# Performance work log

Hardware: AMD Instinct MI355X
Metric: run time of the kernel (lower is better)

The kernel has to match this reference:

```python
import jax, jax.numpy as jnp
import numpy as np

NH, NOPE_D, ROPE_D, V_D, R = 16, 48, 16, 64, 128
EPS = 1e-6

def rms_norm(x, w):
    norm = jax.lax.rsqrt(jnp.mean(jnp.square(x), axis=-1, keepdims=True) + EPS)
    return x * norm * w

def apply_rope(x, cos, sin):
    # x: (..., rope_d); cos/sin broadcastable (..., rope_d//2)
    d = x.shape[-1]
    x1, x2 = x[..., : d // 2], x[..., d // 2 :]
    return jnp.concatenate([x1 * cos - x2 * sin, x2 * cos + x1 * sin], axis=-1)

def setup_inputs() -> dict:
    key = jax.random.key(0)
    ks = jax.random.split(key, 8)
    B, T, D = 2, 2048, 1024
    s = lambda fan_in: 1.0 / np.sqrt(fan_in)
    return {
        "x": jax.random.normal(ks[0], (B, T, D), jnp.float32),
        "cos": jax.random.uniform(ks[1], (T, ROPE_D // 2), jnp.float32),
        "sin": jax.random.uniform(ks[2], (T, ROPE_D // 2), jnp.float32),
        "Wq": jax.random.normal(ks[3], (NH * (NOPE_D + ROPE_D), D), jnp.float32) * s(D),
        "q_norm_w": jnp.ones((NOPE_D + ROPE_D,), jnp.float32),
        "Wkva": jax.random.normal(ks[4], (R + ROPE_D, D), jnp.float32) * s(D),
        "kva_norm_w": jnp.ones((R,), jnp.float32),
        "Wkvb": jax.random.normal(ks[5], (NH * (NOPE_D + V_D), R), jnp.float32) * s(R),
        "Wo": jax.random.normal(ks[6], (D, NH * V_D), jnp.float32) * s(NH * V_D),
    }

def reference(x, cos, sin, Wq, q_norm_w, Wkva, kva_norm_w, Wkvb, Wo):
    B, T, D = x.shape
    # Q path: project, per-head RMSNorm over (nope+rope) dims, split
    q = (x @ Wq.T).reshape(B, T, NH, NOPE_D + ROPE_D)
    q = rms_norm(q, q_norm_w)
    q_nope, q_rope = q[..., :NOPE_D], q[..., NOPE_D:]
    # Low-rank KV path
    kv_a = x @ Wkva.T  # (B,T,R+ROPE_D)
    kv_latent = rms_norm(kv_a[..., :R], kva_norm_w)
    k_rope_raw = kv_a[..., R:]  # (B,T,ROPE_D) shared across heads
    kv_b = (kv_latent @ Wkvb.T).reshape(B, T, NH, NOPE_D + V_D)
    k_nope, v = kv_b[..., :NOPE_D], kv_b[..., NOPE_D:]
    # Decoupled RoPE
    cos_t = cos[None, :T, None, :]  # (1,T,1,rope_d/2)
    sin_t = sin[None, :T, None, :]
    q_rope = apply_rope(q_rope, cos_t, sin_t)
    k_rope = apply_rope(k_rope_raw[:, :, None, :], cos[None, :T, None, :], sin[None, :T, None, :])
    k_rope = jnp.broadcast_to(k_rope, (B, T, NH, ROPE_D))
    q_full = jnp.concatenate([q_nope, q_rope], axis=-1)  # (B,T,NH,64)
    k_full = jnp.concatenate([k_nope, k_rope], axis=-1)
    # Causal attention, scale = 1/sqrt(nope+rope)
    scale = (NOPE_D + ROPE_D) ** -0.5
    scores = jnp.einsum("bqhd,bkhd->bhqk", q_full, k_full) * scale
    causal = jnp.tril(jnp.ones((T, T), bool))
    scores = jnp.where(causal[None, None], scores, -jnp.inf)
    attn = jax.nn.softmax(scores, axis=-1)
    out = jnp.einsum("bhqk,bkhd->bqhd", attn, v).reshape(B, T, NH * V_D)
    return out @ Wo.T
```

## Files before the change

### kernel.cpp

```cpp
#include <hip/hip_runtime.h>
#include <hip/hip_bf16.h>
#include <math.h>

#define NH 16
#define T_ 2048
#define B_ 2
#define D_ 1024
#define EPS 1e-6f

typedef __attribute__((ext_vector_type(8))) short bf16x8;
typedef __attribute__((ext_vector_type(4))) float f32x4;

__device__ __forceinline__ float wred_sum(float v){
  #pragma unroll
  for (int o = 32; o > 0; o >>= 1) v += __shfl_xor(v, o, 64);
  return v;
}

__device__ __forceinline__ unsigned pack_bf16(float a, float b){
  __hip_bfloat162 t = __float22bfloat162_rn(make_float2(a, b));
  unsigned r; __builtin_memcpy(&r, &t, 4); return r;
}

__device__ __forceinline__ void gload_lds16(const void* g, void* l){
  __builtin_amdgcn_global_load_lds((const __attribute__((address_space(1))) void*)g,
                                   (__attribute__((address_space(3))) void*)l, 16, 0, 0);
}

__global__ __launch_bounds__(256)
void cvt5(const float* __restrict__ x, const float* __restrict__ wq,
          const float* __restrict__ wkva, const float* __restrict__ wkvb,
          const float* __restrict__ wo,
          __hip_bfloat16* __restrict__ xb, __hip_bfloat16* __restrict__ wqb,
          __hip_bfloat16* __restrict__ wkvab, __hip_bfloat16* __restrict__ wkvbb,
          __hip_bfloat16* __restrict__ wob)
{
  const int i = blockIdx.x * 256 + threadIdx.x;
  const float* s; __hip_bfloat16* d; size_t soff, doff;
  if      (i < 1048576) { s = x;    d = xb;    soff = doff = i; }
  else if (i < 1310720) { s = wq;   d = wqb;   soff = doff = i - 1048576; }
  else if (i < 1347584) { s = wkva; d = wkvab; soff = doff = i - 1310720; }
  else if (i < 1404928) {
    const int off = i - 1347584;
    const int srow = off >> 5, c4 = off & 31;
    const int h = srow / 112, dd = srow % 112;
    const int drow = (dd < 48) ? (h*48 + dd) : (768 + h*64 + (dd - 48));
    s = wkvb; d = wkvbb; soff = off; doff = (size_t)drow*32 + c4;
  }
  else                  { s = wo;   d = wob;   soff = doff = i - 1404928; }
  float4 v = *(const float4*)(s + soff * 4);
  *(__hip_bfloat162*)(d + doff * 4)     = __float22bfloat162_rn(make_float2(v.x, v.y));
  *(__hip_bfloat162*)(d + doff * 4 + 2) = __float22bfloat162_rn(make_float2(v.z, v.w));
}

template<typename CT>
__global__ __launch_bounds__(256, 2)
void gemm_bt64(const __hip_bfloat16* __restrict__ A, const __hip_bfloat16* __restrict__ W,
               CT* __restrict__ C, int M, int N, int K)
{
  __shared__ __hip_bfloat16 As[2][128 * 64];
  __shared__ __hip_bfloat16 Ws[2][64 * 64];
  const int tid = threadIdx.x;
  const int wv = tid >> 6, lane = tid & 63;
  const int m = lane & 15, quad = lane >> 4;
  const int bm = blockIdx.y * 128, bn = blockIdx.x * 64;

  const __hip_bfloat16* ga[4];
  const __hip_bfloat16* gw[2];
  #pragma unroll
  for (int i = 0; i < 4; i++) {
    const int slot = i*256 + tid;
    const int row = slot >> 3, cb = slot & 7;
    ga[i] = A + (size_t)(bm + row) * K + ((cb ^ (row & 7)) << 3);
  }
  #pragma unroll
  for (int i = 0; i < 2; i++) {
    const int slot = i*256 + tid;
    const int row = slot >> 3, cb = slot & 7;
    int wr = bn + row; if (wr >= N) wr = N - 1;
    gw[i] = W + (size_t)wr * K + ((cb ^ (row & 7)) << 3);
  }
  auto stage = [&](int buf){
    #pragma unroll
    for (int i = 0; i < 4; i++) { gload_lds16(ga[i], &As[buf][(i*256 + wv*64)*8]); ga[i] += 64; }
    #pragma unroll
    for (int i = 0; i < 2; i++) { gload_lds16(gw[i], &Ws[buf][(i*256 + wv*64)*8]); gw[i] += 64; }
  };

  f32x4 acc[2][4];
  #pragma unroll
  for (int mi = 0; mi < 2; mi++)
    #pragma unroll
    for (int nj = 0; nj < 4; nj++) acc[mi][nj] = (f32x4){0.f,0.f,0.f,0.f};

  stage(0);
  const int iters = K >> 6;
  for (int it = 0; it < iters; it++) {
    const int cur = it & 1;
    __syncthreads();
    if (it + 1 < iters) stage(cur ^ 1);
    #pragma unroll
    for (int ks = 0; ks < 2; ks++) {
      const int cb = ((ks*4 + quad) ^ (m & 7)) << 3;
      bf16x8 af[2], wf[4];
      #pragma unroll
      for (int mi = 0; mi < 2; mi++)
        af[mi] = *(const bf16x8*)(&As[cur][(wv*32 + mi*16 + m) * 64 + cb]);
      #pragma unroll
      for (int nj = 0; nj < 4; nj++)
        wf[nj] = *(const bf16x8*)(&Ws[cur][(nj*16 + m) * 64 + cb]);
      #pragma unroll
      for (int mi = 0; mi < 2; mi++)
        #pragma unroll
        for (int nj = 0; nj < 4; nj++)
          acc[mi][nj] = __builtin_amdgcn_mfma_f32_16x16x32_bf16(af[mi], wf[nj], acc[mi][nj], 0, 0, 0);
    }
  }

  #pragma unroll
  for (int mi = 0; mi < 2; mi++)
    #pragma unroll
    for (int nj = 0; nj < 4; nj++) {
      const int col = bn + nj*16 + m;
      if (col < N) {
        #pragma unroll
        for (int r = 0; r < 4; r++) {
          const int row = bm + wv*32 + mi*16 + quad*4 + r;
          if constexpr (sizeof(CT) == 2)
            C[(size_t)row * N + col] = (CT)__float2bfloat16(acc[mi][nj][r]);
          else
            C[(size_t)row * N + col] = acc[mi][nj][r];
        }
      }
    }
}

__global__ __launch_bounds__(256, 2)
void gemm_qkva(const __hip_bfloat16* __restrict__ A, const __hip_bfloat16* __restrict__ Wqb,
               const __hip_bfloat16* __restrict__ Wkvab,
               const float* __restrict__ qw, const float* __restrict__ cosp,
               const float* __restrict__ sinp,
               __hip_bfloat16* __restrict__ qb, float* __restrict__ kva)
{
  __shared__ __hip_bfloat16 As[2][128 * 64];
  __shared__ __hip_bfloat16 Ws[2][64 * 64];
  const int K = 1024;
  const int tid = threadIdx.x;
  const int wv = tid >> 6, lane = tid & 63;
  const int m = lane & 15, quad = lane >> 4;
  const int bm = blockIdx.y * 128;
  const bool isq = blockIdx.x < 16;
  const __hip_bfloat16* W = isq ? Wqb : Wkvab;
  const int bn = isq ? blockIdx.x*64 : (blockIdx.x - 16)*64;
  const int Nw = isq ? 1024 : 144;

  const __hip_bfloat16* ga[4];
  const __hip_bfloat16* gw[2];
  #pragma unroll
  for (int i = 0; i < 4; i++) {
    const int slot = i*256 + tid;
    const int row = slot >> 3, cb = slot & 7;
    ga[i] = A + (size_t)(bm + row) * K + ((cb ^ (row & 7)) << 3);
  }
  #pragma unroll
  for (int i = 0; i < 2; i++) {
    const int slot = i*256 + tid;
    const int row = slot >> 3, cb = slot & 7;
    int wr = bn + row; if (wr >= Nw) wr = Nw - 1;
    gw[i] = W + (size_t)wr * K + ((cb ^ (row & 7)) << 3);
  }
  auto stage = [&](int buf){
    #pragma unroll
    for (int i = 0; i < 4; i++) { gload_lds16(ga[i], &As[buf][(i*256 + wv*64)*8]); ga[i] += 64; }
    #pragma unroll
    for (int i = 0; i < 2; i++) { gload_lds16(gw[i], &Ws[buf][(i*256 + wv*64)*8]); gw[i] += 64; }
  };

  f32x4 acc[2][4];
  #pragma unroll
  for (int mi = 0; mi < 2; mi++)
    #pragma unroll
    for (int nj = 0; nj < 4; nj++) acc[mi][nj] = (f32x4){0.f,0.f,0.f,0.f};

  stage(0);
  for (int it = 0; it < 16; it++) {
    const int cur = it & 1;
    __syncthreads();
    if (it < 15) stage(cur ^ 1);
    #pragma unroll
    for (int ks = 0; ks < 2; ks++) {
      const int cb = ((ks*4 + quad) ^ (m & 7)) << 3;
      bf16x8 af[2], wf[4];
      #pragma unroll
      for (int mi = 0; mi < 2; mi++)
        af[mi] = *(const bf16x8*)(&As[cur][(wv*32 + mi*16 + m) * 64 + cb]);
      #pragma unroll
      for (int nj = 0; nj < 4; nj++)
        wf[nj] = *(const bf16x8*)(&Ws[cur][(nj*16 + m) * 64 + cb]);
      #pragma unroll
      for (int mi = 0; mi < 2; mi++)
        #pragma unroll
        for (int nj = 0; nj < 4; nj++)
          acc[mi][nj] = __builtin_amdgcn_mfma_f32_16x16x32_bf16(af[mi], wf[nj], acc[mi][nj], 0, 0, 0);
    }
  }

  if (isq) {
    const int head = blockIdx.x;
    float qwv[4];
    #pragma unroll
    for (int nj = 0; nj < 4; nj++) qwv[nj] = qw[nj*16 + m];
    const int j = m & 7;
    #pragma unroll
    for (int mi = 0; mi < 2; mi++) {
      #pragma unroll
      for (int r = 0; r < 4; r++) {
        float ss = 0.f;
        #pragma unroll
        for (int nj = 0; nj < 4; nj++) { const float t = acc[mi][nj][r]; ss = fmaf(t, t, ss); }
        ss += __shfl_xor(ss, 1, 64); ss += __shfl_xor(ss, 2, 64);
        ss += __shfl_xor(ss, 4, 64); ss += __shfl_xor(ss, 8, 64);
        const float nrm = rsqrtf(ss * (1.0f/64.0f) + EPS);
        float v[4];
        #pragma unroll
        for (int nj = 0; nj < 4; nj++) v[nj] = acc[mi][nj][r] * nrm * qwv[nj];
        const int grow = bm + wv*32 + mi*16 + quad*4 + r;
        const int t = grow & (T_ - 1);
        const int b = grow >> 11;
        const float part = __shfl_xor(v[3], 8, 64);
        const float c = cosp[t*8 + j], sn = sinp[t*8 + j];
        v[3] = (m < 8) ? (v[3]*c - part*sn) : (v[3]*c + part*sn);
        __hip_bfloat16* dst = qb + ((size_t)(b*NH + head)*T_ + t)*64 + m;
        #pragma unroll
        for (int nj = 0; nj < 4; nj++) dst[nj*16] = __float2bfloat16(v[nj] * 0.125f);
      }
    }
  } else {
    #pragma unroll
    for (int mi = 0; mi < 2; mi++)
      #pragma unroll
      for (int nj = 0; nj < 4; nj++) {
        const int col = bn + nj*16 + m;
        if (col < 144) {
          #pragma unroll
          for (int r = 0; r < 4; r++) {
            const int row = bm + wv*32 + mi*16 + quad*4 + r;
            kva[(size_t)row * 144 + col] = acc[mi][nj][r];
          }
        }
      }
  }
}

__global__ void prep_kv(const float* __restrict__ kva, const float* __restrict__ kw,
                        const float* __restrict__ cosp, const float* __restrict__ sinp,
                        __hip_bfloat16* __restrict__ kvl16, __hip_bfloat16* __restrict__ krope16)
{
  const int tid = threadIdx.x;
  const int bt = blockIdx.x;
  const int t = bt % T_;
  const float* row = kva + (size_t)bt * 144;
  const float v = row[tid];
  float s = wred_sum(v * v);
  __shared__ float red[2];
  if ((tid & 63) == 0) red[tid >> 6] = s;
  __syncthreads();
  const float total = red[0] + red[1];
  const float norm = rsqrtf(total * (1.0f/128.0f) + EPS);
  kvl16[(size_t)bt * 128 + tid] = __float2bfloat16(v * norm * kw[tid]);
  if (tid < 16) {
    const int j = tid & 7;
    const float c = cosp[t*8 + j], sn = sinp[t*8 + j];
    const float x1 = row[128 + j], x2 = row[136 + j];
    krope16[(size_t)bt * 16 + tid] = __float2bfloat16((tid < 8) ? (x1 * c - x2 * sn)
                                                               : (x2 * c + x1 * sn));
  }
}

__global__ __launch_bounds__(256, 2)
void gemm_kvb(const __hip_bfloat16* __restrict__ A, const __hip_bfloat16* __restrict__ W,
              __hip_bfloat16* __restrict__ knope, __hip_bfloat16* __restrict__ vt)
{
  __shared__ __hip_bfloat16 As[2][128 * 64];
  __shared__ __hip_bfloat16 Ws[2][64 * 64];
  const int K = 128;
  const int tid = threadIdx.x;
  const int wv = tid >> 6, lane = tid & 63;
  const int m = lane & 15, quad = lane >> 4;
  const int bm = blockIdx.y * 128, bn = blockIdx.x * 64;

  const __hip_bfloat16* ga[4];
  const __hip_bfloat16* gw[2];
  #pragma unroll
  for (int i = 0; i < 4; i++) {
    const int slot = i*256 + tid;
    const int row = slot >> 3, cb = slot & 7;
    ga[i] = A + (size_t)(bm + row) * K + ((cb ^ (row & 7)) << 3);
  }
  #pragma unroll
  for (int i = 0; i < 2; i++) {
    const int slot = i*256 + tid;
    const int row = slot >> 3, cb = slot & 7;
    gw[i] = W + (size_t)(bn + row) * K + ((cb ^ (row & 7)) << 3);
  }
  auto stage = [&](int buf){
    #pragma unroll
    for (int i = 0; i < 4; i++) { gload_lds16(ga[i], &As[buf][(i*256 + wv*64)*8]); ga[i] += 64; }
    #pragma unroll
    for (int i = 0; i < 2; i++) { gload_lds16(gw[i], &Ws[buf][(i*256 + wv*64)*8]); gw[i] += 64; }
  };

  f32x4 acc[2][4];
  #pragma unroll
  for (int mi = 0; mi < 2; mi++)
    #pragma unroll
    for (int nj = 0; nj < 4; nj++) acc[mi][nj] = (f32x4){0.f,0.f,0.f,0.f};

  stage(0);
  for (int it = 0; it < 2; it++) {
    const int cur = it & 1;
    __syncthreads();
    if (it == 0) stage(1);
    #pragma unroll
    for (int ks = 0; ks < 2; ks++) {
      const int cb = ((ks*4 + quad) ^ (m & 7)) << 3;
      bf16x8 af[2], wf[4];
      #pragma unroll
      for (int mi = 0; mi < 2; mi++)
        af[mi] = *(const bf16x8*)(&As[cur][(wv*32 + mi*16 + m) * 64 + cb]);
      #pragma unroll
      for (int nj = 0; nj < 4; nj++)
        wf[nj] = *(const bf16x8*)(&Ws[cur][(nj*16 + m) * 64 + cb]);
      #pragma unroll
      for (int mi = 0; mi < 2; mi++)
        #pragma unroll
        for (int nj = 0; nj < 4; nj++)
          acc[mi][nj] = __builtin_amdgcn_mfma_f32_16x16x32_bf16(af[mi], wf[nj], acc[mi][nj], 0, 0, 0);
    }
  }

  if (bn < 768) {
    #pragma unroll
    for (int mi = 0; mi < 2; mi++)
      #pragma unroll
      for (int nj = 0; nj < 4; nj++) {
        const int col = bn + nj*16 + m;
        #pragma unroll
        for (int r = 0; r < 4; r++) {
          const int row = bm + wv*32 + mi*16 + quad*4 + r;
          knope[(size_t)row * 768 + col] = __float2bfloat16(acc[mi][nj][r]);
        }
      }
  } else {
    __syncthreads();
    short* TL = (short*)&As[0][0];
    #pragma unroll
    for (int mi = 0; mi < 2; mi++)
      #pragma unroll
      for (int nj = 0; nj < 4; nj++) {
        const int d = nj*16 + m;
        #pragma unroll
        for (int r = 0; r < 4; r++) {
          const int tl = wv*32 + mi*16 + quad*4 + r;
          __hip_bfloat16 hv = __float2bfloat16(acc[mi][nj][r]);
          short sv; __builtin_memcpy(&sv, &hv, 2);
          TL[d*136 + tl] = sv;
        }
      }
    __syncthreads();
    const int h = (bn - 768) >> 6;
    const int b = bm >> 11;
    const int t0 = bm & (T_ - 1);
    #pragma unroll
    for (int i = 0; i < 4; i++) {
      const int unit = i*256 + tid;
      const int d = unit >> 4, tu = unit & 15;
      *(bf16x8*)(vt + ((size_t)(b*NH + h)*64 + d)*T_ + t0 + tu*8)
          = *(const bf16x8*)(TL + d*136 + tu*8);
    }
  }
}

__device__ __forceinline__ void fa_softmax(f32x4 (&s)[8], const bool diag,
    const int k0, const int qglob, const int m, const int quad,
    float& mrun, float& lrun, f32x4 (&o)[4], bf16x8 (&a)[4])
{
  if (diag) {
    #pragma unroll
    for (int sub = 0; sub < 8; sub++)
      #pragma unroll
      for (int r = 0; r < 4; r++)
        if (k0 + sub*16 + quad*4 + r > qglob) s[sub][r] = -1e30f;
  }
  float tm = -3.0e38f;
  #pragma unroll
  for (int sub = 0; sub < 8; sub++)
    #pragma unroll
    for (int r = 0; r < 4; r++) tm = fmaxf(tm, s[sub][r]);
  tm = fmaxf(tm, __shfl_xor(tm, 16, 64));
  tm = fmaxf(tm, __shfl_xor(tm, 32, 64));
  const float mn = fmaxf(mrun, tm);
  const float alpha = __expf(mrun - mn);
  float rs = 0.f;
  float p[8][4];
  #pragma unroll
  for (int sub = 0; sub < 8; sub++)
    #pragma unroll
    for (int r = 0; r < 4; r++) {
      const float e = __expf(s[sub][r] - mn);
      p[sub][r] = e; rs += e;
    }
  rs += __shfl_xor(rs, 16, 64);
  rs += __shfl_xor(rs, 32, 64);
  lrun = lrun * alpha + rs;
  mrun = mn;

  unsigned u[8][2];
  #pragma unroll
  for (int sub = 0; sub < 8; sub++) {
    u[sub][0] = pack_bf16(p[sub][0], p[sub][1]);
    u[sub][1] = pack_bf16(p[sub][2], p[sub][3]);
  }
  #pragma unroll
  for (int c = 0; c < 4; c++) {
    union { int i[4]; bf16x8 v; } au;
    #pragma unroll
    for (int w4 = 0; w4 < 4; w4++) {
      const int src = (((2*quad + (w4 >> 1)) & 3) << 4) | m;
      const int lo = __shfl((int)u[c*2][w4 & 1], src, 64);
      const int hi = __shfl((int)u[c*2+1][w4 & 1], src, 64);
      au.i[w4] = (quad & 2) ? hi : lo;
    }
    a[c] = au.v;
  }

  float al[4];
  #pragma unroll
  for (int r = 0; r < 4; r++) al[r] = __shfl(alpha, (quad << 2) | r, 64);
  #pragma unroll
  for (int vs = 0; vs < 4; vs++)
    #pragma unroll
    for (int r = 0; r < 4; r++) o[vs][r] *= al[r];
}

__device__ __forceinline__ void fa_store(float lrun, f32x4 (&oacc)[4],
    const int b, const int qrow0, const int h, const int m, const int quad,
    __hip_bfloat16* __restrict__ aout)
{
  float lr[4];
  #pragma unroll
  for (int r = 0; r < 4; r++) lr[r] = __shfl(lrun, (quad << 2) | r, 64);
  #pragma unroll
  for (int vs = 0; vs < 4; vs++)
    #pragma unroll
    for (int r = 0; r < 4; r++)
      aout[(size_t)(b*T_ + qrow0 + quad*4 + r) * 1024 + h*64 + vs*16 + m]
          = __float2bfloat16(oacc[vs][r] / lr[r]);
}

__global__ __launch_bounds__(256, 2)
void attn_pair2(const __hip_bfloat16* __restrict__ qb,
                const __hip_bfloat16* __restrict__ knope,
                const __hip_bfloat16* __restrict__ krope16,
                const __hip_bfloat16* __restrict__ vt16,
                __hip_bfloat16* __restrict__ aout)
{
  __shared__ __hip_bfloat16 SL[32768];
  const int tid = threadIdx.x;
  const int wv = tid >> 6, lane = tid & 63;
  const int m = lane & 15, quad = lane >> 4;
  const int ta = blockIdx.x;
  const int tb = 31 - ta;
  const int bh = blockIdx.y;
  const int b = bh >> 4, h = bh & 15;
  const int qbaseA = ta*64 + wv*16;
  const int qbaseB = tb*64 + wv*16;
  const int ntA = (ta + 2) >> 1;
  const int ntB = (tb + 2) >> 1;

  const __hip_bfloat16* qra = qb + ((size_t)bh*T_ + qbaseA + m)*64 + quad*8;
  const bf16x8 qA0 = *(const bf16x8*)qra, qA1 = *(const bf16x8*)(qra + 32);
  const __hip_bfloat16* qrb = qb + ((size_t)bh*T_ + qbaseB + m)*64 + quad*8;
  const bf16x8 qB0 = *(const bf16x8*)qrb, qB1 = *(const bf16x8*)(qrb + 32);

  const __hip_bfloat16* pK[4]; size_t iK[4];
  const __hip_bfloat16* pV[4];
  #pragma unroll
  for (int i = 0; i < 4; i++) {
    const int slot = i*256 + tid;
    const int krow = slot >> 3;
    const int kde = (slot & 7) ^ (krow & 7);
    if (kde < 6) { pK[i] = knope + (size_t)(b*T_ + krow)*768 + h*48 + kde*8; iK[i] = (size_t)128*768; }
    else         { pK[i] = krope16 + (size_t)(b*T_ + krow)*16 + (kde-6)*8;   iK[i] = (size_t)128*16; }
    const int vd = slot >> 4;
    const int vde = (slot & 15) ^ (vd & 7);
    pV[i] = vt16 + ((size_t)bh*64 + vd)*T_ + vde*8;
  }

  auto stage = [&](int buf){
    #pragma unroll
    for (int i = 0; i < 4; i++) {
      gload_lds16(pK[i], SL + buf*8192 + (i*256 + wv*64)*8);
      gload_lds16(pV[i], SL + 16384 + buf*8192 + (i*256 + wv*64)*8);
      pK[i] += iK[i]; pV[i] += 128;
    }
  };

  f32x4 oA[4], oB[4];
  #pragma unroll
  for (int vs = 0; vs < 4; vs++) { oA[vs] = (f32x4){0.f,0.f,0.f,0.f}; oB[vs] = (f32x4){0.f,0.f,0.f,0.f}; }
  float mA = -3.0e38f, lA = 0.f, mB = -3.0e38f, lB = 0.f;

  const int sw0 = quad ^ (m & 7);
  stage(0);

  for (int kt = 0; kt < ntB; kt++) {
    const int cur = kt & 1;
    __syncthreads();
    const __hip_bfloat16* Kc = SL + cur*8192;
    const __hip_bfloat16* Vc = SL + 16384 + cur*8192;
    const bool doA = (kt < ntA);

    f32x4 sA[8], sB[8];
    #pragma unroll
    for (int sub = 0; sub < 8; sub++) {
      const bf16x8 kf0 = *(const bf16x8*)(Kc + (sub*16 + m)*64 + sw0*8);
      const bf16x8 kf1 = *(const bf16x8*)(Kc + (sub*16 + m)*64 + (sw0^4)*8);
      f32x4 z = (f32x4){0.f,0.f,0.f,0.f};
      z = __builtin_amdgcn_mfma_f32_16x16x32_bf16(kf0, qB0, z, 0, 0, 0);
      z = __builtin_amdgcn_mfma_f32_16x16x32_bf16(kf1, qB1, z, 0, 0, 0);
      sB[sub] = z;
      if (doA) {
        f32x4 y = (f32x4){0.f,0.f,0.f,0.f};
        y = __builtin_amdgcn_mfma_f32_16x16x32_bf16(kf0, qA0, y, 0, 0, 0);
        y = __builtin_amdgcn_mfma_f32_16x16x32_bf16(kf1, qA1, y, 0, 0, 0);
        sA[sub] = y;
      }
    }

    if (kt + 1 < ntB) stage(cur ^ 1);

    bf16x8 aA[4], aB[4];
    fa_softmax(sB, kt == ntB-1, kt*128, qbaseB + m, m, quad, mB, lB, oB, aB);
    if (doA) fa_softmax(sA, kt == ntA-1, kt*128, qbaseA + m, m, quad, mA, lA, oA, aA);

    #pragma unroll
    for (int vs = 0; vs < 4; vs++) {
      #pragma unroll
      for (int c = 0; c < 4; c++) {
        const bf16x8 vf = *(const bf16x8*)(Vc + (vs*16 + m)*128 + (((c*4 + quad) ^ (m & 7)) << 3));
        oB[vs] = __builtin_amdgcn_mfma_f32_16x16x32_bf16(aB[c], vf, oB[vs], 0, 0, 0);
        if (doA) oA[vs] = __builtin_amdgcn_mfma_f32_16x16x32_bf16(aA[c], vf, oA[vs], 0, 0, 0);
      }
    }
  }

  fa_store(lA, oA, b, qbaseA, h, m, quad, aout);
  fa_store(lB, oB, b, qbaseB, h, m, quad, aout);
}

extern "C" void kernel_launch(void* const* d_in, const int* in_sizes, int n_in,
                              void* d_out, int out_size, void* d_ws, size_t ws_size,
                              hipStream_t stream)
{
  const float* x    = (const float*)d_in[0];
  const float* cosp = (const float*)d_in[1];
  const float* sinp = (const float*)d_in[2];
  const float* Wq   = (const float*)d_in[3];
  const float* qw   = (const float*)d_in[4];
  const float* Wkva = (const float*)d_in[5];
  const float* kw   = (const float*)d_in[6];
  const float* Wkvb = (const float*)d_in[7];
  const float* Wo   = (const float*)d_in[8];
  float* out = (float*)d_out;

  float* kva = (float*)d_ws;
  __hip_bfloat16* xb16    = (__hip_bfloat16*)(kva + 589824);
  __hip_bfloat16* knope16 = xb16 + 4194304;
  __hip_bfloat16* kvl16   = knope16 + 3145728;
  __hip_bfloat16* qb16    = kvl16 + 524288;
  __hip_bfloat16* vt16    = qb16 + 4194304;
  __hip_bfloat16* krope16 = vt16 + 4194304;
  __hip_bfloat16* Wqb     = krope16 + 65536;
  __hip_bfloat16* Wkvab   = Wqb + 1048576;
  __hip_bfloat16* Wkvbb   = Wkvab + 147456;
  __hip_bfloat16* Wob     = Wkvbb + 229376;
  __hip_bfloat16* ab16    = Wob + 1048576;

  const int M = B_ * T_;

  cvt5<<<6512, 256, 0, stream>>>(x, Wq, Wkva, Wkvb, Wo, xb16, Wqb, Wkvab, Wkvbb, Wob);
  gemm_qkva<<<dim3(19, 32), 256, 0, stream>>>(xb16, Wqb, Wkvab, qw, cosp, sinp, qb16, kva);
  prep_kv<<<M, 128, 0, stream>>>(kva, kw, cosp, sinp, kvl16, krope16);
  gemm_kvb<<<dim3(28, 32), 256, 0, stream>>>(kvl16, Wkvbb, knope16, vt16);
  attn_pair2<<<dim3(16, B_ * NH), 256, 0, stream>>>(qb16, knope16, krope16, vt16, ab16);
  gemm_bt64<float><<<dim3(16, 32), 256, 0, stream>>>(ab16, Wob, out, M, 1024, 1024);
}
```

Baseline: 190.8 us.

## Enlarge GEMM tiles to 128x128, use exp2 softmax and MFMA row sums

The Q/KV-A projection and output GEMMs now use 128x128 block tiles, with each wave computing a 64x64 sub-tile. This gives more operand reuse per LDS load and halves the grid size. The attention softmax folds log2(e) into the Q scale so it can call exp2f. The per-row sum is now built by an extra MFMA against a ones vector instead of shuffle reductions. The trade-offs are higher accumulator register pressure, fewer blocks to fill the CUs, and extra MFMA work in the attention loop.

```diff
diff --git a/kernel.cpp b/kernel.cpp
--- a/kernel.cpp
+++ b/kernel.cpp
@@ -55,41 +55,38 @@
 
 template<typename CT>
 __global__ __launch_bounds__(256, 2)
-void gemm_bt64(const __hip_bfloat16* __restrict__ A, const __hip_bfloat16* __restrict__ W,
-               CT* __restrict__ C, int M, int N, int K)
+void gemm_bt128(const __hip_bfloat16* __restrict__ A, const __hip_bfloat16* __restrict__ W,
+                CT* __restrict__ C, int M, int N, int K)
 {
   __shared__ __hip_bfloat16 As[2][128 * 64];
-  __shared__ __hip_bfloat16 Ws[2][64 * 64];
+  __shared__ __hip_bfloat16 Ws[2][128 * 64];
   const int tid = threadIdx.x;
   const int wv = tid >> 6, lane = tid & 63;
   const int m = lane & 15, quad = lane >> 4;
-  const int bm = blockIdx.y * 128, bn = blockIdx.x * 64;
+  const int bm = blockIdx.y * 128, bn = blockIdx.x * 128;
+  const int wm = wv >> 1, wn = wv & 1;
 
   const __hip_bfloat16* ga[4];
-  const __hip_bfloat16* gw[2];
+  const __hip_bfloat16* gw[4];
   #pragma unroll
   for (int i = 0; i < 4; i++) {
     const int slot = i*256 + tid;
     const int row = slot >> 3, cb = slot & 7;
     ga[i] = A + (size_t)(bm + row) * K + ((cb ^ (row & 7)) << 3);
-  }
-  #pragma unroll
-  for (int i = 0; i < 2; i++) {
-    const int slot = i*256 + tid;
-    const int row = slot >> 3, cb = slot & 7;
     int wr = bn + row; if (wr >= N) wr = N - 1;
     gw[i] = W + (size_t)wr * K + ((cb ^ (row & 7)) << 3);
   }
   auto stage = [&](int buf){
     #pragma unroll
-    for (int i = 0; i < 4; i++) { gload_lds16(ga[i], &As[buf][(i*256 + wv*64)*8]); ga[i] += 64; }
-    #pragma unroll
-    for (int i = 0; i < 2; i++) { gload_lds16(gw[i], &Ws[buf][(i*256 + wv*64)*8]); gw[i] += 64; }
+    for (int i = 0; i < 4; i++) {
+      gload_lds16(ga[i], &As[buf][(i*256 + wv*64)*8]); ga[i] += 64;
+      gload_lds16(gw[i], &Ws[buf][(i*256 + wv*64)*8]); gw[i] += 64;
+    }
   };
 
-  f32x4 acc[2][4];
-  #pragma unroll
-  for (int mi = 0; mi < 2; mi++)
+  f32x4 acc[4][4];
+  #pragma unroll
+  for (int mi = 0; mi < 4; mi++)
     #pragma unroll
     for (int nj = 0; nj < 4; nj++) acc[mi][nj] = (f32x4){0.f,0.f,0.f,0.f};
 
@@ -102,15 +99,15 @@
     #pragma unroll
     for (int ks = 0; ks < 2; ks++) {
       const int cb = ((ks*4 + quad) ^ (m & 7)) << 3;
-      bf16x8 af[2], wf[4];
-      #pragma unroll
-      for (int mi = 0; mi < 2; mi++)
-        af[mi] = *(const bf16x8*)(&As[cur][(wv*32 + mi*16 + m) * 64 + cb]);
+      bf16x8 af[4], wf[4];
+      #pragma unroll
+      for (int mi = 0; mi < 4; mi++)
+        af[mi] = *(const bf16x8*)(&As[cur][(wm*64 + mi*16 + m) * 64 + cb]);
       #pragma unroll
       for (int nj = 0; nj < 4; nj++)
-        wf[nj] = *(const bf16x8*)(&Ws[cur][(nj*16 + m) * 64 + cb]);
-      #pragma unroll
-      for (int mi = 0; mi < 2; mi++)
+        wf[nj] = *(const bf16x8*)(&Ws[cur][(wn*64 + nj*16 + m) * 64 + cb]);
+      #pragma unroll
+      for (int mi = 0; mi < 4; mi++)
         #pragma unroll
         for (int nj = 0; nj < 4; nj++)
           acc[mi][nj] = __builtin_amdgcn_mfma_f32_16x16x32_bf16(af[mi], wf[nj], acc[mi][nj], 0, 0, 0);
@@ -118,14 +115,14 @@
   }
 
   #pragma unroll
-  for (int mi = 0; mi < 2; mi++)
+  for (int mi = 0; mi < 4; mi++)
     #pragma unroll
     for (int nj = 0; nj < 4; nj++) {
-      const int col = bn + nj*16 + m;
+      const int col = bn + wn*64 + nj*16 + m;
       if (col < N) {
         #pragma unroll
         for (int r = 0; r < 4; r++) {
-          const int row = bm + wv*32 + mi*16 + quad*4 + r;
+          const int row = bm + wm*64 + mi*16 + quad*4 + r;
           if constexpr (sizeof(CT) == 2)
             C[(size_t)row * N + col] = (CT)__float2bfloat16(acc[mi][nj][r]);
           else
@@ -143,42 +140,39 @@
                __hip_bfloat16* __restrict__ qb, float* __restrict__ kva)
 {
   __shared__ __hip_bfloat16 As[2][128 * 64];
-  __shared__ __hip_bfloat16 Ws[2][64 * 64];
+  __shared__ __hip_bfloat16 Ws[2][128 * 64];
   const int K = 1024;
   const int tid = threadIdx.x;
   const int wv = tid >> 6, lane = tid & 63;
   const int m = lane & 15, quad = lane >> 4;
   const int bm = blockIdx.y * 128;
-  const bool isq = blockIdx.x < 16;
+  const int wm = wv >> 1, wn = wv & 1;
+  const bool isq = blockIdx.x < 8;
   const __hip_bfloat16* W = isq ? Wqb : Wkvab;
-  const int bn = isq ? blockIdx.x*64 : (blockIdx.x - 16)*64;
+  const int bn = isq ? blockIdx.x*128 : (blockIdx.x - 8)*128;
   const int Nw = isq ? 1024 : 144;
 
   const __hip_bfloat16* ga[4];
-  const __hip_bfloat16* gw[2];
+  const __hip_bfloat16* gw[4];
   #pragma unroll
   for (int i = 0; i < 4; i++) {
     const int slot = i*256 + tid;
     const int row = slot >> 3, cb = slot & 7;
     ga[i] = A + (size_t)(bm + row) * K + ((cb ^ (row & 7)) << 3);
-  }
-  #pragma unroll
-  for (int i = 0; i < 2; i++) {
-    const int slot = i*256 + tid;
-    const int row = slot >> 3, cb = slot & 7;
     int wr = bn + row; if (wr >= Nw) wr = Nw - 1;
     gw[i] = W + (size_t)wr * K + ((cb ^ (row & 7)) << 3);
   }
   auto stage = [&](int buf){
     #pragma unroll
-    for (int i = 0; i < 4; i++) { gload_lds16(ga[i], &As[buf][(i*256 + wv*64)*8]); ga[i] += 64; }
-    #pragma unroll
-    for (int i = 0; i < 2; i++) { gload_lds16(gw[i], &Ws[buf][(i*256 + wv*64)*8]); gw[i] += 64; }
+    for (int i = 0; i < 4; i++) {
+      gload_lds16(ga[i], &As[buf][(i*256 + wv*64)*8]); ga[i] += 64;
+      gload_lds16(gw[i], &Ws[buf][(i*256 + wv*64)*8]); gw[i] += 64;
+    }
   };
 
-  f32x4 acc[2][4];
-  #pragma unroll
-  for (int mi = 0; mi < 2; mi++)
+  f32x4 acc[4][4];
+  #pragma unroll
+  for (int mi = 0; mi < 4; mi++)
     #pragma unroll
     for (int nj = 0; nj < 4; nj++) acc[mi][nj] = (f32x4){0.f,0.f,0.f,0.f};
 
@@ -190,15 +184,15 @@
     #pragma unroll
     for (int ks = 0; ks < 2; ks++) {
       const int cb = ((ks*4 + quad) ^ (m & 7)) << 3;
-      bf16x8 af[2], wf[4];
-      #pragma unroll
-      for (int mi = 0; mi < 2; mi++)
-        af[mi] = *(const bf16x8*)(&As[cur][(wv*32 + mi*16 + m) * 64 + cb]);
+      bf16x8 af[4], wf[4];
+      #pragma unroll
+      for (int mi = 0; mi < 4; mi++)
+        af[mi] = *(const bf16x8*)(&As[cur][(wm*64 + mi*16 + m) * 64 + cb]);
       #pragma unroll
       for (int nj = 0; nj < 4; nj++)
-        wf[nj] = *(const bf16x8*)(&Ws[cur][(nj*16 + m) * 64 + cb]);
-      #pragma unroll
-      for (int mi = 0; mi < 2; mi++)
+        wf[nj] = *(const bf16x8*)(&Ws[cur][(wn*64 + nj*16 + m) * 64 + cb]);
+      #pragma unroll
+      for (int mi = 0; mi < 4; mi++)
         #pragma unroll
         for (int nj = 0; nj < 4; nj++)
           acc[mi][nj] = __builtin_amdgcn_mfma_f32_16x16x32_bf16(af[mi], wf[nj], acc[mi][nj], 0, 0, 0);
@@ -206,13 +200,14 @@
   }
 
   if (isq) {
-    const int head = blockIdx.x;
+    const int head = blockIdx.x*2 + wn;
     float qwv[4];
     #pragma unroll
     for (int nj = 0; nj < 4; nj++) qwv[nj] = qw[nj*16 + m];
     const int j = m & 7;
-    #pragma unroll
-    for (int mi = 0; mi < 2; mi++) {
+    const float qscale = 0.125f * 1.44269504f;
+    #pragma unroll
+    for (int mi = 0; mi < 4; mi++) {
       #pragma unroll
       for (int r = 0; r < 4; r++) {
         float ss = 0.f;
@@ -224,7 +219,7 @@
         float v[4];
         #pragma unroll
         for (int nj = 0; nj < 4; nj++) v[nj] = acc[mi][nj][r] * nrm * qwv[nj];
-        const int grow = bm + wv*32 + mi*16 + quad*4 + r;
+        const int grow = bm + wm*64 + mi*16 + quad*4 + r;
         const int t = grow & (T_ - 1);
         const int b = grow >> 11;
         const float part = __shfl_xor(v[3], 8, 64);
@@ -232,19 +227,19 @@
         v[3] = (m < 8) ? (v[3]*c - part*sn) : (v[3]*c + part*sn);
         __hip_bfloat16* dst = qb + ((size_t)(b*NH + head)*T_ + t)*64 + m;
         #pragma unroll
-        for (int nj = 0; nj < 4; nj++) dst[nj*16] = __float2bfloat16(v[nj] * 0.125f);
+        for (int nj = 0; nj < 4; nj++) dst[nj*16] = __float2bfloat16(v[nj] * qscale);
       }
     }
   } else {
     #pragma unroll
-    for (int mi = 0; mi < 2; mi++)
+    for (int mi = 0; mi < 4; mi++)
       #pragma unroll
       for (int nj = 0; nj < 4; nj++) {
-        const int col = bn + nj*16 + m;
+        const int col = bn + wn*64 + nj*16 + m;
         if (col < 144) {
           #pragma unroll
           for (int r = 0; r < 4; r++) {
-            const int row = bm + wv*32 + mi*16 + quad*4 + r;
+            const int row = bm + wm*64 + mi*16 + quad*4 + r;
             kva[(size_t)row * 144 + col] = acc[mi][nj][r];
           }
         }
@@ -383,7 +378,7 @@
 
 __device__ __forceinline__ void fa_softmax(f32x4 (&s)[8], const bool diag,
     const int k0, const int qglob, const int m, const int quad,
-    float& mrun, float& lrun, f32x4 (&o)[4], bf16x8 (&a)[4])
+    float& mrun, f32x4 (&o)[4], f32x4& lacc, bf16x8 (&a)[4])
 {
   if (diag) {
     #pragma unroll
@@ -400,19 +395,13 @@
   tm = fmaxf(tm, __shfl_xor(tm, 16, 64));
   tm = fmaxf(tm, __shfl_xor(tm, 32, 64));
   const float mn = fmaxf(mrun, tm);
-  const float alpha = __expf(mrun - mn);
-  float rs = 0.f;
+  const float alpha = exp2f(mrun - mn);
   float p[8][4];
   #pragma unroll
   for (int sub = 0; sub < 8; sub++)
     #pragma unroll
-    for (int r = 0; r < 4; r++) {
-      const float e = __expf(s[sub][r] - mn);
-      p[sub][r] = e; rs += e;
-    }
-  rs += __shfl_xor(rs, 16, 64);
-  rs += __shfl_xor(rs, 32, 64);
-  lrun = lrun * alpha + rs;
+    for (int r = 0; r < 4; r++)
+      p[sub][r] = exp2f(s[sub][r] - mn);
   mrun = mn;
 
   unsigned u[8][2];
@@ -441,15 +430,17 @@
   for (int vs = 0; vs < 4; vs++)
     #pragma unroll
     for (int r = 0; r < 4; r++) o[vs][r] *= al[r];
-}
-
-__device__ __forceinline__ void fa_store(float lrun, f32x4 (&oacc)[4],
+  #pragma unroll
+  for (int r = 0; r < 4; r++) lacc[r] *= al[r];
+}
+
+__device__ __forceinline__ void fa_store(const f32x4& lacc, f32x4 (&oacc)[4],
     const int b, const int qrow0, const int h, const int m, const int quad,
     __hip_bfloat16* __restrict__ aout)
 {
   float lr[4];
   #pragma unroll
-  for (int r = 0; r < 4; r++) lr[r] = __shfl(lrun, (quad << 2) | r, 64);
+  for (int r = 0; r < 4; r++) lr[r] = __shfl(lacc[r], quad << 4, 64);
   #pragma unroll
   for (int vs = 0; vs < 4; vs++)
     #pragma unroll
@@ -483,6 +474,11 @@
   const __hip_bfloat16* qrb = qb + ((size_t)bh*T_ + qbaseB + m)*64 + quad*8;
   const bf16x8 qB0 = *(const bf16x8*)qrb, qB1 = *(const bf16x8*)(qrb + 32);
 
+  union { short e[8]; bf16x8 v; } onesu;
+  #pragma unroll
+  for (int j = 0; j < 8; j++) onesu.e[j] = (m == 0) ? (short)0x3F80 : (short)0;
+  const bf16x8 vones = onesu.v;
+
   const __hip_bfloat16* pK[4]; size_t iK[4];
   const __hip_bfloat16* pV[4];
   #pragma unroll
@@ -509,7 +505,8 @@
   f32x4 oA[4], oB[4];
   #pragma unroll
   for (int vs = 0; vs < 4; vs++) { oA[vs] = (f32x4){0.f,0.f,0.f,0.f}; oB[vs] = (f32x4){0.f,0.f,0.f,0.f}; }
-  float mA = -3.0e38f, lA = 0.f, mB = -3.0e38f, lB = 0.f;
+  f32x4 lA = (f32x4){0.f,0.f,0.f,0.f}, lB = (f32x4){0.f,0.f,0.f,0.f};
+  float mA = -3.0e38f, mB = -3.0e38f;
 
   const int sw0 = quad ^ (m & 7);
   stage(0);
@@ -541,9 +538,14 @@
     if (kt + 1 < ntB) stage(cur ^ 1);
 
     bf16x8 aA[4], aB[4];
-    fa_softmax(sB, kt == ntB-1, kt*128, qbaseB + m, m, quad, mB, lB, oB, aB);
-    if (doA) fa_softmax(sA, kt == ntA-1, kt*128, qbaseA + m, m, quad, mA, lA, oA, aA);
-
+    fa_softmax(sB, kt == ntB-1, kt*128, qbaseB + m, m, quad, mB, oB, lB, aB);
+    if (doA) fa_softmax(sA, kt == ntA-1, kt*128, qbaseA + m, m, quad, mA, oA, lA, aA);
+
+    #pragma unroll
+    for (int c = 0; c < 4; c++) {
+      lB = __builtin_amdgcn_mfma_f32_16x16x32_bf16(aB[c], vones, lB, 0, 0, 0);
+      if (doA) lA = __builtin_amdgcn_mfma_f32_16x16x32_bf16(aA[c], vones, lA, 0, 0, 0);
+    }
     #pragma unroll
     for (int vs = 0; vs < 4; vs++) {
       #pragma unroll
@@ -590,9 +592,9 @@
   const int M = B_ * T_;
 
   cvt5<<<6512, 256, 0, stream>>>(x, Wq, Wkva, Wkvb, Wo, xb16, Wqb, Wkvab, Wkvbb, Wob);
-  gemm_qkva<<<dim3(19, 32), 256, 0, stream>>>(xb16, Wqb, Wkvab, qw, cosp, sinp, qb16, kva);
+  gemm_qkva<<<dim3(10, 32), 256, 0, stream>>>(xb16, Wqb, Wkvab, qw, cosp, sinp, qb16, kva);
   prep_kv<<<M, 128, 0, stream>>>(kva, kw, cosp, sinp, kvl16, krope16);
   gemm_kvb<<<dim3(28, 32), 256, 0, stream>>>(kvl16, Wkvbb, knope16, vt16);
   attn_pair2<<<dim3(16, B_ * NH), 256, 0, stream>>>(qb16, knope16, krope16, vt16, ab16);
-  gemm_bt64<float><<<dim3(16, 32), 256, 0, stream>>>(ab16, Wob, out, M, 1024, 1024);
-}
+  gemm_bt128<float><<<dim3(8, 32), 256, 0, stream>>>(ab16, Wob, out, M, 1024, 1024);
+}
```

Result: slower. 202.8 us (+6.3%).
